# Kernel tuning notes

Measured on AMD Instinct MI355X. Metric: run time of the kernel, lower is better.

Reference implementation:

```python
import jax, jax.numpy as jnp
import numpy as np

PS = 2      # patch_size
TOPK = 3    # topk


def setup_inputs() -> dict:
    key = jax.random.key(0)
    x = jax.random.normal(key, (16, 128, 64, 64), dtype=jnp.float32)
    alpha = jnp.asarray(5.0, dtype=jnp.float32)
    return {"x": x, "alpha": alpha}


def reference(x, alpha):
    ps = PS
    b, c, h, w = x.shape
    nph, npw = h // ps, w // ps
    npatch = nph * npw
    pa = ps * ps
    # F.normalize(x, p=2, dim=-3): L2-normalize over channels
    nrm = jnp.sqrt(jnp.sum(x * x, axis=1, keepdims=True))
    x = x / jnp.maximum(nrm, 1e-12)
    # patchify: [b,c,h,w] -> [b,c,num_patches,patch_area]
    x = x.reshape(b * c * nph, ps, npw, ps)
    x = jnp.swapaxes(x, 1, 2).reshape(b, c, npatch, pa)
    diag = np.arange(ps) * (ps + 1)          # diagonal positions within a patch
    x = x[:, :, :, diag]                     # [b,c,npatch,ps]
    x = jnp.swapaxes(x, 1, 3)                # [b,ps,npatch,c]
    # per-diagonal-pixel patch correlation matrix
    corr = jnp.einsum('bpnc,bpmc->bpnm', x, x)           # [b,ps,np,np]
    avg = jnp.mean(corr, axis=1, keepdims=True)
    corr = jnp.concatenate([corr, avg], axis=1)          # [b,ps+1,np,np]
    # gaussian self-suppression mask (1 - gaussian centered at each patch)
    rat_s = 0.05
    sr, sc = nph * rat_s, npw * rat_s
    ind_r = jnp.arange(nph, dtype=jnp.float32).reshape(1, nph, 1)
    ind_c = jnp.arange(npw, dtype=jnp.float32).reshape(1, 1, npw)
    cr, cc = jnp.meshgrid(jnp.arange(nph, dtype=jnp.float32),
                          jnp.arange(npw, dtype=jnp.float32), indexing='ij')
    cent_r = cr.reshape(npatch, 1, 1)
    cent_c = cc.reshape(npatch, 1, 1)
    g = jnp.exp(-(ind_r - cent_r) ** 2 / (2.0 * sr * sr)) \
        * jnp.exp(-(ind_c - cent_c) ** 2 / (2.0 * sc * sc))   # [np,nph,npw]
    mask = (1.0 - g).reshape(1, 1, npatch, npatch)
    s = (corr * mask) * alpha
    # dual (row + column) softmax
    a = jax.nn.softmax(s, axis=-1) * jax.nn.softmax(s, axis=-2)  # [b,ps+1,np,np]
    # scatter: diagonal in-patch pixels get their own map, rest get the avg map
    src = np.full(pa, ps, dtype=np.int64)
    src[diag] = np.arange(ps)
    a = a[:, src]                              # [b,pa,np,np]
    # un-patchify attention back to [b, npatch, h, w]
    a = jnp.swapaxes(a, 1, 3)                  # [b,np,np,pa]
    a = a.reshape(b * npatch * nph, npw, ps, ps)
    a = jnp.swapaxes(a, 1, 2)
    a = a.reshape(b, npatch, h, w)
    # top-k over the patch (correlation-source) dim
    vals = jax.lax.top_k(jnp.moveaxis(a, 1, -1), TOPK)[0]  # [b,h,w,k]
    return jnp.moveaxis(vals, -1, 1)           # [b,k,h,w]
```

## Files before the change

### kernel.cpp

```cpp
#include <hip/hip_runtime.h>
#include <math.h>

#define NB 16
#define NCH 128
#define NH 64
#define NW 64
#define NP 1024

#define TN 32
#define TM 128
#define KC 32
#define KP 36
#define PK 40

#define NTILE 144

typedef __attribute__((ext_vector_type(8))) short short8v;
typedef __attribute__((ext_vector_type(4))) float f32x4;

__device__ __forceinline__ float med3(float a, float b, float c) {
  return __builtin_amdgcn_fmed3f(a, b, c);
}
__device__ __forceinline__ void top3_ins(float& t0, float& t1, float& t2, float a) {
  float n0 = fmaxf(t0, a);
  float n1 = med3(a, t0, t1);
  float n2 = med3(a, t1, t2);
  t0 = n0; t1 = n1; t2 = n2;
}
__device__ __forceinline__ float dot4(float4 a, float4 b) {
  return a.x * b.x + a.y * b.y + a.z * b.z + a.w * b.w;
}
__device__ __forceinline__ ushort f2bf(float f) {
  unsigned u = __float_as_uint(f);
  unsigned r = (u + 0x7FFFu + ((u >> 16) & 1u)) >> 16;
  return (ushort)r;
}
__device__ __forceinline__ float bf2f(ushort h) {
  return __uint_as_float(((unsigned)h) << 16);
}
__device__ __forceinline__ int tile_base(int g) {
  return 32 * g - 2 * g * (g - 1);
}

__global__ __launch_bounds__(256) void prep_split(const float* __restrict__ x,
                                                  ushort* __restrict__ Vs,
                                                  float* __restrict__ rsum) {
  int blk = blockIdx.x;
  int t = threadIdx.x;
  int gid = blk * 256 + t;
  if (gid < NB * 3 * NP) rsum[gid] = 0.f;

  int b = blk >> 5;
  int c = (blk >> 4) & 1;
  int ng = blk & 15;
  int nl = t >> 2;
  int kq = t & 3;
  int n = ng * 64 + nl;
  int i = 2 * (n >> 5) + c;
  int j = 2 * (n & 31) + c;
  const float* xp = x + (size_t)b * NCH * NH * NW + i * NW + j;

  float v[32];
#pragma unroll
  for (int e = 0; e < 32; ++e)
    v[e] = xp[(size_t)(kq * 32 + e) * NH * NW];

  float ss = 0.f;
#pragma unroll
  for (int e = 0; e < 32; ++e) ss += v[e] * v[e];
  ss += __shfl_xor(ss, 1, 64);
  ss += __shfl_xor(ss, 2, 64);
  float r = 1.0f / fmaxf(sqrtf(ss), 1e-12f);

  size_t base = ((size_t)(b * 2 + c) * 3) * NP * NCH + (size_t)n * NCH + kq * 32;
  ushort* p1 = Vs + base;
  ushort* p2 = Vs + base + (size_t)NP * NCH;
  ushort* p3 = Vs + base + (size_t)2 * NP * NCH;
#pragma unroll
  for (int kg2 = 0; kg2 < 4; ++kg2) {
    ushort h1[8], h2[8], h3[8];
#pragma unroll
    for (int e = 0; e < 8; ++e) {
      float vv = v[kg2 * 8 + e] * r;
      ushort a = f2bf(vv);
      float r1 = vv - bf2f(a);
      ushort bq = f2bf(r1);
      float r2 = r1 - bf2f(bq);
      ushort cq = f2bf(r2);
      h1[e] = a; h2[e] = bq; h3[e] = cq;
    }
    *(float4*)(p1 + kg2 * 8) = *(float4*)h1;
    *(float4*)(p2 + kg2 * 8) = *(float4*)h2;
    *(float4*)(p3 + kg2 * 8) = *(float4*)h3;
  }
}

__global__ __launch_bounds__(256, 4) void gemm_mfma(
    const ushort* __restrict__ Vs, const float* __restrict__ alpha_p,
    float2* __restrict__ Sbuf, float* __restrict__ rsum) {
  __shared__ __align__(16) char smem[3 * 32 * PK * 2 + 3 * 128 * PK * 2];
  ushort (*A_s)[32][PK] = reinterpret_cast<ushort(*)[32][PK]>(smem);
  ushort (*B_s)[128][PK] =
      reinterpret_cast<ushort(*)[128][PK]>(smem + 3 * 32 * PK * 2);

  int wg = blockIdx.x;
  int xcd = wg & 7;
  int jj = wg >> 3;
  int half = (jj >= NTILE) ? 1 : 0;
  const int b = 2 * xcd + half;
  int id = jj - half * NTILE;
  const int tid0 = id;
  int g = 0;
  while (id >= 4 * (8 - g)) { id -= 4 * (8 - g); ++g; }
  const int ni = 4 * g + id / (8 - g);
  const int mj = g + id % (8 - g);
  const int n0 = ni * TN;
  const int m0 = mj * TM;

  const int t = threadIdx.x;
  const int lane = t & 63, wv = t >> 6;
  const int jc = lane & 15, kg = lane >> 4;
  const float alpha = *alpha_p;
  const ushort* Vsb = Vs + (size_t)b * 6 * NP * NCH;
  float* rs = rsum + (size_t)b * 3 * NP;

  f32x4 acc[2][2][2];
#pragma unroll
  for (int c = 0; c < 2; ++c)
#pragma unroll
    for (int i = 0; i < 2; ++i)
#pragma unroll
      for (int j = 0; j < 2; ++j) acc[c][i][j] = (f32x4){0.f, 0.f, 0.f, 0.f};

#pragma unroll
  for (int c = 0; c < 2; ++c) {
    for (int k0 = 0; k0 < NCH; k0 += KC) {
      __syncthreads();
#pragma unroll
      for (int q = 0; q < 2; ++q) {
        int flat = q * 256 + t;
        if (flat < 384) {
          int p = flat >> 7;
          int rem = flat & 127;
          int row = rem >> 2, u = rem & 3;
          const ushort* src = Vsb + ((size_t)(c * 3 + p) * NP + n0 + row) * NCH + k0 + u * 8;
          *(float4*)&A_s[p][row][u * 8] = *(const float4*)src;
        }
      }
#pragma unroll
      for (int q = 0; q < 6; ++q) {
        int flat = q * 256 + t;
        int p = flat >> 9;
        int rem = flat & 511;
        int row = rem >> 2, u = rem & 3;
        const ushort* src = Vsb + ((size_t)(c * 3 + p) * NP + m0 + row) * NCH + k0 + u * 8;
        *(float4*)&B_s[p][row][u * 8] = *(const float4*)src;
      }
      __syncthreads();

      short8v a1n0 = *(const short8v*)&A_s[0][jc][kg * 8];
      short8v a1n1 = *(const short8v*)&A_s[0][16 + jc][kg * 8];
      short8v a2n0 = *(const short8v*)&A_s[1][jc][kg * 8];
      short8v a2n1 = *(const short8v*)&A_s[1][16 + jc][kg * 8];
      short8v a3n0 = *(const short8v*)&A_s[2][jc][kg * 8];
      short8v a3n1 = *(const short8v*)&A_s[2][16 + jc][kg * 8];
      {
        short8v b0 = *(const short8v*)&B_s[0][wv * 32 + jc][kg * 8];
        short8v b1 = *(const short8v*)&B_s[0][wv * 32 + 16 + jc][kg * 8];
        acc[c][0][0] = __builtin_amdgcn_mfma_f32_16x16x32_bf16(a1n0, b0, acc[c][0][0], 0, 0, 0);
        acc[c][1][0] = __builtin_amdgcn_mfma_f32_16x16x32_bf16(a1n1, b0, acc[c][1][0], 0, 0, 0);
        acc[c][0][1] = __builtin_amdgcn_mfma_f32_16x16x32_bf16(a1n0, b1, acc[c][0][1], 0, 0, 0);
        acc[c][1][1] = __builtin_amdgcn_mfma_f32_16x16x32_bf16(a1n1, b1, acc[c][1][1], 0, 0, 0);
        acc[c][0][0] = __builtin_amdgcn_mfma_f32_16x16x32_bf16(a2n0, b0, acc[c][0][0], 0, 0, 0);
        acc[c][1][0] = __builtin_amdgcn_mfma_f32_16x16x32_bf16(a2n1, b0, acc[c][1][0], 0, 0, 0);
        acc[c][0][1] = __builtin_amdgcn_mfma_f32_16x16x32_bf16(a2n0, b1, acc[c][0][1], 0, 0, 0);
        acc[c][1][1] = __builtin_amdgcn_mfma_f32_16x16x32_bf16(a2n1, b1, acc[c][1][1], 0, 0, 0);
        acc[c][0][0] = __builtin_amdgcn_mfma_f32_16x16x32_bf16(a3n0, b0, acc[c][0][0], 0, 0, 0);
        acc[c][1][0] = __builtin_amdgcn_mfma_f32_16x16x32_bf16(a3n1, b0, acc[c][1][0], 0, 0, 0);
        acc[c][0][1] = __builtin_amdgcn_mfma_f32_16x16x32_bf16(a3n0, b1, acc[c][0][1], 0, 0, 0);
        acc[c][1][1] = __builtin_amdgcn_mfma_f32_16x16x32_bf16(a3n1, b1, acc[c][1][1], 0, 0, 0);
      }
      {
        short8v b0 = *(const short8v*)&B_s[1][wv * 32 + jc][kg * 8];
        short8v b1 = *(const short8v*)&B_s[1][wv * 32 + 16 + jc][kg * 8];
        acc[c][0][0] = __builtin_amdgcn_mfma_f32_16x16x32_bf16(a1n0, b0, acc[c][0][0], 0, 0, 0);
        acc[c][1][0] = __builtin_amdgcn_mfma_f32_16x16x32_bf16(a1n1, b0, acc[c][1][0], 0, 0, 0);
        acc[c][0][1] = __builtin_amdgcn_mfma_f32_16x16x32_bf16(a1n0, b1, acc[c][0][1], 0, 0, 0);
        acc[c][1][1] = __builtin_amdgcn_mfma_f32_16x16x32_bf16(a1n1, b1, acc[c][1][1], 0, 0, 0);
        acc[c][0][0] = __builtin_amdgcn_mfma_f32_16x16x32_bf16(a2n0, b0, acc[c][0][0], 0, 0, 0);
        acc[c][1][0] = __builtin_amdgcn_mfma_f32_16x16x32_bf16(a2n1, b0, acc[c][1][0], 0, 0, 0);
        acc[c][0][1] = __builtin_amdgcn_mfma_f32_16x16x32_bf16(a2n0, b1, acc[c][0][1], 0, 0, 0);
        acc[c][1][1] = __builtin_amdgcn_mfma_f32_16x16x32_bf16(a2n1, b1, acc[c][1][1], 0, 0, 0);
      }
      {
        short8v b0 = *(const short8v*)&B_s[2][wv * 32 + jc][kg * 8];
        short8v b1 = *(const short8v*)&B_s[2][wv * 32 + 16 + jc][kg * 8];
        acc[c][0][0] = __builtin_amdgcn_mfma_f32_16x16x32_bf16(a1n0, b0, acc[c][0][0], 0, 0, 0);
        acc[c][1][0] = __builtin_amdgcn_mfma_f32_16x16x32_bf16(a1n1, b0, acc[c][1][0], 0, 0, 0);
        acc[c][0][1] = __builtin_amdgcn_mfma_f32_16x16x32_bf16(a1n0, b1, acc[c][0][1], 0, 0, 0);
        acc[c][1][1] = __builtin_amdgcn_mfma_f32_16x16x32_bf16(a1n1, b1, acc[c][1][1], 0, 0, 0);
      }
    }
  }

  float e[2][4][3];
  float gcol[2][3];
#pragma unroll
  for (int ns = 0; ns < 2; ++ns)
#pragma unroll
    for (int r = 0; r < 4; ++r)
#pragma unroll
      for (int c = 0; c < 3; ++c) e[ns][r][c] = 0.f;
#pragma unroll
  for (int ms = 0; ms < 2; ++ms)
#pragma unroll
    for (int c = 0; c < 3; ++c) gcol[ms][c] = 0.f;

#pragma unroll
  for (int ns = 0; ns < 2; ++ns) {
#pragma unroll
    for (int r = 0; r < 4; ++r) {
      int nl = ns * 16 + kg * 4 + r;
      int n = n0 + nl;
      int nr = n >> 5, nc = n & 31;
      float2* rowp = Sbuf + ((size_t)(b * NTILE + tid0) * 32 + nl) * TM;
#pragma unroll
      for (int ms = 0; ms < 2; ++ms) {
        int ml = wv * 32 + ms * 16 + jc;
        int m = m0 + ml;
        int dr = nr - (m >> 5);
        int dc = nc - (m & 31);
        float gss = __expf(-(float)(dr * dr + dc * dc) * 0.1953125f);
        float wgt = (1.0f - gss) * alpha;
        float s0 = acc[0][ns][ms][r] * wgt;
        float s1 = acc[1][ns][ms][r] * wgt;
        float e0 = __expf(s0);
        float e1 = __expf(s1);
        float e2 = __expf(0.5f * (s0 + s1));
        if (m >= n) {
          rowp[ml] = make_float2(s0, s1);
          e[ns][r][0] += e0; e[ns][r][1] += e1; e[ns][r][2] += e2;
        }
        if (m > n) { gcol[ms][0] += e0; gcol[ms][1] += e1; gcol[ms][2] += e2; }
      }
    }
  }
#pragma unroll
  for (int off = 1; off < 16; off <<= 1) {
#pragma unroll
    for (int ns = 0; ns < 2; ++ns)
#pragma unroll
      for (int r = 0; r < 4; ++r)
#pragma unroll
        for (int c = 0; c < 3; ++c)
          e[ns][r][c] += __shfl_xor(e[ns][r][c], off, 64);
  }
  if (jc == 0) {
#pragma unroll
    for (int ns = 0; ns < 2; ++ns)
#pragma unroll
      for (int r = 0; r < 4; ++r)
#pragma unroll
        for (int c = 0; c < 3; ++c)
          atomicAdd(&rs[(size_t)c * NP + (n0 + ns * 16 + kg * 4 + r)], e[ns][r][c]);
  }
#pragma unroll
  for (int off = 16; off < 64; off <<= 1) {
#pragma unroll
    for (int ms = 0; ms < 2; ++ms)
#pragma unroll
      for (int c = 0; c < 3; ++c)
        gcol[ms][c] += __shfl_xor(gcol[ms][c], off, 64);
  }
  if (kg == 0) {
#pragma unroll
    for (int ms = 0; ms < 2; ++ms) {
      int m = m0 + wv * 32 + ms * 16 + jc;
#pragma unroll
      for (int c = 0; c < 3; ++c)
        atomicAdd(&rs[(size_t)c * NP + m], gcol[ms][c]);
    }
  }
}

__global__ __launch_bounds__(256) void recip_kernel(float* __restrict__ p, int nelem) {
  int i = blockIdx.x * 256 + threadIdx.x;
  if (i < nelem) p[i] = 1.0f / p[i];
}

__global__ __launch_bounds__(256, 4) void tile_topk(
    const float2* __restrict__ Sbuf, const float* __restrict__ rinv,
    float* __restrict__ P) {
  __shared__ float2 tile[32][129];

  const int b = blockIdx.y;
  int id = blockIdx.x;
  const int tid0 = id;
  int g = 0;
  while (id >= 4 * (8 - g)) { id -= 4 * (8 - g); ++g; }
  const int ni = 4 * g + id / (8 - g);
  const int mj = g + id % (8 - g);
  const int n0 = ni * TN;
  const int m0 = mj * TM;

  const int t = threadIdx.x;
  const float* rb = rinv + (size_t)b * 3 * NP;
  const float2* src = Sbuf + (size_t)(b * NTILE + tid0) * 32 * TM;
  float* Pp = P + ((size_t)(b * NTILE + tid0) * 160) * 9;

#pragma unroll
  for (int q = 0; q < 16; ++q) {
    int flat = q * 256 + t;
    int row = flat >> 7;
    int colu = flat & 127;
    tile[row][colu] = src[row * TM + colu];
  }
  __syncthreads();

  {
    int rl = t >> 3;
    int c0 = (t & 7) * 16;
    int n = n0 + rl;
    float rin0 = rb[(size_t)0 * NP + n];
    float rin1 = rb[(size_t)1 * NP + n];
    float rin2 = rb[(size_t)2 * NP + n];
    float t0[3] = {0.f, 0.f, 0.f}, t1[3] = {0.f, 0.f, 0.f}, t2[3] = {0.f, 0.f, 0.f};
#pragma unroll
    for (int cc = 0; cc < 16; ++cc) {
      int ml = c0 + cc;
      int m = m0 + ml;
      if (m >= n) {
        float2 sv = tile[rl][ml];
        float a0 = __expf(2.0f * sv.x) * rin0 * rb[(size_t)0 * NP + m];
        float a1 = __expf(2.0f * sv.y) * rin1 * rb[(size_t)1 * NP + m];
        float a2 = __expf(sv.x + sv.y) * rin2 * rb[(size_t)2 * NP + m];
        top3_ins(t0[0], t1[0], t2[0], a0);
        top3_ins(t0[1], t1[1], t2[1], a1);
        top3_ins(t0[2], t1[2], t2[2], a2);
      }
    }
#pragma unroll
    for (int off = 1; off < 8; off <<= 1) {
#pragma unroll
      for (int c = 0; c < 3; ++c) {
        float o0 = __shfl_xor(t0[c], off, 64);
        float o1 = __shfl_xor(t1[c], off, 64);
        float o2 = __shfl_xor(t2[c], off, 64);
        top3_ins(t0[c], t1[c], t2[c], o0);
        top3_ins(t0[c], t1[c], t2[c], o1);
        top3_ins(t0[c], t1[c], t2[c], o2);
      }
    }
    if ((t & 7) == 0) {
#pragma unroll
      for (int c = 0; c < 3; ++c) {
        Pp[(size_t)rl * 9 + c * 3 + 0] = t0[c];
        Pp[(size_t)rl * 9 + c * 3 + 1] = t1[c];
        Pp[(size_t)rl * 9 + c * 3 + 2] = t2[c];
      }
    }
  }

  {
    int cu = t >> 1;
    int r0 = (t & 1) * 16;
    int m = m0 + cu;
    float rim0 = rb[(size_t)0 * NP + m];
    float rim1 = rb[(size_t)1 * NP + m];
    float rim2 = rb[(size_t)2 * NP + m];
    float t0[3] = {0.f, 0.f, 0.f}, t1[3] = {0.f, 0.f, 0.f}, t2[3] = {0.f, 0.f, 0.f};
#pragma unroll
    for (int rr = 0; rr < 16; ++rr) {
      int row = r0 + rr;
      int n = n0 + row;
      if (n < m) {
        float2 sv = tile[row][cu];
        float a0 = __expf(2.0f * sv.x) * rim0 * rb[(size_t)0 * NP + n];
        float a1 = __expf(2.0f * sv.y) * rim1 * rb[(size_t)1 * NP + n];
        float a2 = __expf(sv.x + sv.y) * rim2 * rb[(size_t)2 * NP + n];
        top3_ins(t0[0], t1[0], t2[0], a0);
        top3_ins(t0[1], t1[1], t2[1], a1);
        top3_ins(t0[2], t1[2], t2[2], a2);
      }
    }
#pragma unroll
    for (int c = 0; c < 3; ++c) {
      float o0 = __shfl_xor(t0[c], 1, 64);
      float o1 = __shfl_xor(t1[c], 1, 64);
      float o2 = __shfl_xor(t2[c], 1, 64);
      top3_ins(t0[c], t1[c], t2[c], o0);
      top3_ins(t0[c], t1[c], t2[c], o1);
      top3_ins(t0[c], t1[c], t2[c], o2);
    }
    if ((t & 1) == 0) {
#pragma unroll
      for (int c = 0; c < 3; ++c) {
        Pp[(size_t)(32 + cu) * 9 + c * 3 + 0] = t0[c];
        Pp[(size_t)(32 + cu) * 9 + c * 3 + 1] = t1[c];
        Pp[(size_t)(32 + cu) * 9 + c * 3 + 2] = t2[c];
      }
    }
  }
}

__global__ __launch_bounds__(256) void merge_kernel(
    const float* __restrict__ P, float* __restrict__ out) {
  int gid = blockIdx.x * 256 + threadIdx.x;
  int n = gid & (NP - 1);
  int tmp = gid >> 10;
  int c = tmp % 3;
  int b = tmp / 3;

  const float* Pb = P + (size_t)b * NTILE * 160 * 9;
  int g = n >> 7;
  int ni = n >> 5;
  int nl = n & 31;
  int ml = n & 127;

  float u0 = 0.f, u1 = 0.f, u2 = 0.f;
  int rbase = tile_base(g) + (ni - 4 * g) * (8 - g) - g;
  for (int mj = g; mj < 8; ++mj) {
    const float* p = Pb + ((size_t)(rbase + mj) * 160 + nl) * 9 + c * 3;
    top3_ins(u0, u1, u2, p[0]);
    top3_ins(u0, u1, u2, p[1]);
    top3_ins(u0, u1, u2, p[2]);
  }
  for (int nii = 0; nii <= 4 * g + 3; ++nii) {
    int gg = nii >> 2;
    int tid = tile_base(gg) + (nii - 4 * gg) * (8 - gg) + (g - gg);
    const float* p = Pb + ((size_t)tid * 160 + 32 + ml) * 9 + c * 3;
    top3_ins(u0, u1, u2, p[0]);
    top3_ins(u0, u1, u2, p[1]);
    top3_ins(u0, u1, u2, p[2]);
  }

  int pr = n >> 5, pc = n & 31;
  int ii0, jj0, ii1 = -1, jj1 = -1;
  if (c == 0)      { ii0 = 2 * pr;     jj0 = 2 * pc; }
  else if (c == 1) { ii0 = 2 * pr + 1; jj0 = 2 * pc + 1; }
  else             { ii0 = 2 * pr;     jj0 = 2 * pc + 1;
                     ii1 = 2 * pr + 1; jj1 = 2 * pc; }
  out[(((size_t)b * 3 + 0) * NH + ii0) * NW + jj0] = u0;
  out[(((size_t)b * 3 + 1) * NH + ii0) * NW + jj0] = u1;
  out[(((size_t)b * 3 + 2) * NH + ii0) * NW + jj0] = u2;
  if (ii1 >= 0) {
    out[(((size_t)b * 3 + 0) * NH + ii1) * NW + jj1] = u0;
    out[(((size_t)b * 3 + 1) * NH + ii1) * NW + jj1] = u1;
    out[(((size_t)b * 3 + 2) * NH + ii1) * NW + jj1] = u2;
  }
}

__global__ __launch_bounds__(256) void prep_kernel(const float* __restrict__ x,
                                                   float* __restrict__ V) {
  int blk = blockIdx.x;
  int t = threadIdx.x;
  int b = blk >> 3;
  int c = (blk >> 2) & 1;
  int n = (blk & 3) * 256 + t;
  int i = 2 * (n >> 5) + c;
  int j = 2 * (n & 31) + c;
  const float* xp = x + (size_t)b * NCH * NH * NW + i * NW + j;
  float ss = 0.f;
#pragma unroll 8
  for (int ch = 0; ch < NCH; ++ch) {
    float v = xp[(size_t)ch * NH * NW];
    ss += v * v;
  }
  float r = 1.0f / fmaxf(sqrtf(ss), 1e-12f);
  float* vp = V + (((size_t)b * 2 + c) * NP + n) * NCH;
#pragma unroll 8
  for (int ch = 0; ch < NCH; ++ch) {
    vp[ch] = xp[(size_t)ch * NH * NW] * r;
  }
}

template <int PASS>
__global__ __launch_bounds__(256, 2) void corr_kernel(
    const float* __restrict__ V, const float* __restrict__ alpha_p,
    float* __restrict__ rsum_g, float* __restrict__ out) {
  __shared__ __align__(16) float As[2][TN][KP];
  __shared__ __align__(16) float Bs[2][TM][KP];

  const int b = blockIdx.y;
  const int n0 = blockIdx.x * TN;
  const int t = threadIdx.x;
  const int tx = t & 31;
  const int ty = t >> 5;
  const float alpha = *alpha_p;
  const float* Vb = V + (size_t)b * 2 * NP * NCH;

  float sm[3][4];
  float t0[3][4], t1[3][4], t2[3][4];
  float rin[3][4];
#pragma unroll
  for (int c = 0; c < 3; ++c)
#pragma unroll
    for (int i = 0; i < 4; ++i) {
      sm[c][i] = 0.f;
      t0[c][i] = 0.f; t1[c][i] = 0.f; t2[c][i] = 0.f;
    }
  if (PASS == 2) {
#pragma unroll
    for (int c = 0; c < 3; ++c)
#pragma unroll
      for (int i = 0; i < 4; ++i) {
        int n = n0 + ty * 4 + i;
        rin[c][i] = 1.0f / rsum_g[((size_t)b * 3 + c) * NP + n];
      }
  }

  for (int mc = 0; mc < NP / TM; ++mc) {
    const int m0 = mc * TM;
    float acc[2][4][4];
#pragma unroll
    for (int c = 0; c < 2; ++c)
#pragma unroll
      for (int i = 0; i < 4; ++i)
#pragma unroll
        for (int j = 0; j < 4; ++j) acc[c][i][j] = 0.f;

    for (int k0 = 0; k0 < NCH; k0 += KC) {
      __syncthreads();
#pragma unroll
      for (int q = 0; q < 2; ++q) {
        int flat = q * 256 + t;
        int c = flat >> 8;
        int rem = flat & 255;
        int row = rem >> 3;
        int kgx = rem & 7;
        float4 v4 = *(const float4*)(Vb + ((size_t)c * NP + n0 + row) * NCH + k0 + kgx * 4);
        *(float4*)&As[c][row][kgx * 4] = v4;
      }
#pragma unroll
      for (int q = 0; q < 8; ++q) {
        int flat = q * 256 + t;
        int c = flat >> 10;
        int rem = flat & 1023;
        int row = rem >> 3;
        int kgx = rem & 7;
        float4 v4 = *(const float4*)(Vb + ((size_t)c * NP + m0 + row) * NCH + k0 + kgx * 4);
        *(float4*)&Bs[c][row][kgx * 4] = v4;
      }
      __syncthreads();

      for (int kgx = 0; kgx < KC; kgx += 4) {
        float4 a4[2][4], b4[2][4];
#pragma unroll
        for (int c = 0; c < 2; ++c)
#pragma unroll
          for (int i = 0; i < 4; ++i)
            a4[c][i] = *(const float4*)&As[c][ty * 4 + i][kgx];
#pragma unroll
        for (int c = 0; c < 2; ++c)
#pragma unroll
          for (int j = 0; j < 4; ++j)
            b4[c][j] = *(const float4*)&Bs[c][tx + 32 * j][kgx];
#pragma unroll
        for (int c = 0; c < 2; ++c)
#pragma unroll
          for (int i = 0; i < 4; ++i)
#pragma unroll
            for (int j = 0; j < 4; ++j)
              acc[c][i][j] += dot4(a4[c][i], b4[c][j]);
      }
    }

    float rim[3][4];
    if (PASS == 2) {
#pragma unroll
      for (int c = 0; c < 3; ++c)
#pragma unroll
        for (int j = 0; j < 4; ++j) {
          int m = m0 + tx + 32 * j;
          rim[c][j] = 1.0f / rsum_g[((size_t)b * 3 + c) * NP + m];
        }
    }
#pragma unroll
    for (int i = 0; i < 4; ++i) {
      int n = n0 + ty * 4 + i;
      int nr = n >> 5, nc = n & 31;
      float s[3][4];
#pragma unroll
      for (int j = 0; j < 4; ++j) {
        int m = m0 + tx + 32 * j;
        int dr = nr - (m >> 5);
        int dc = nc - (m & 31);
        float gq = __expf(-(float)(dr * dr + dc * dc) * 0.1953125f);
        float wgt = (1.0f - gq) * alpha;
        float s0v = acc[0][i][j] * wgt;
        float s1v = acc[1][i][j] * wgt;
        s[0][j] = s0v; s[1][j] = s1v; s[2][j] = 0.5f * (s0v + s1v);
      }
      if (PASS == 1) {
#pragma unroll
        for (int c = 0; c < 3; ++c) {
          sm[c][i] += __expf(s[c][0]) + __expf(s[c][1]) +
                      __expf(s[c][2]) + __expf(s[c][3]);
        }
      } else {
#pragma unroll
        for (int c = 0; c < 3; ++c) {
#pragma unroll
          for (int j = 0; j < 4; ++j) {
            float a = __expf(2.0f * s[c][j]) * rin[c][i] * rim[c][j];
            top3_ins(t0[c][i], t1[c][i], t2[c][i], a);
          }
        }
      }
    }
  }

  if (PASS == 1) {
#pragma unroll
    for (int off = 1; off < 32; off <<= 1) {
#pragma unroll
      for (int c = 0; c < 3; ++c)
#pragma unroll
        for (int i = 0; i < 4; ++i)
          sm[c][i] += __shfl_xor(sm[c][i], off, 64);
    }
    if (tx == 0) {
#pragma unroll
      for (int c = 0; c < 3; ++c)
#pragma unroll
        for (int i = 0; i < 4; ++i) {
          int n = n0 + ty * 4 + i;
          rsum_g[((size_t)b * 3 + c) * NP + n] = sm[c][i];
        }
    }
  } else {
#pragma unroll
    for (int off = 1; off < 32; off <<= 1) {
#pragma unroll
      for (int c = 0; c < 3; ++c)
#pragma unroll
        for (int i = 0; i < 4; ++i) {
          float o0 = __shfl_xor(t0[c][i], off, 64);
          float o1 = __shfl_xor(t1[c][i], off, 64);
          float o2 = __shfl_xor(t2[c][i], off, 64);
          top3_ins(t0[c][i], t1[c][i], t2[c][i], o0);
          top3_ins(t0[c][i], t1[c][i], t2[c][i], o1);
          top3_ins(t0[c][i], t1[c][i], t2[c][i], o2);
        }
    }
    if (tx == 0) {
#pragma unroll
      for (int c = 0; c < 3; ++c)
#pragma unroll
        for (int i = 0; i < 4; ++i) {
          int n = n0 + ty * 4 + i;
          int pr = n >> 5, pc = n & 31;
          float v0 = t0[c][i], v1 = t1[c][i], v2 = t2[c][i];
          int ii0, jj0, ii1 = -1, jj1 = -1;
          if (c == 0)      { ii0 = 2 * pr;     jj0 = 2 * pc; }
          else if (c == 1) { ii0 = 2 * pr + 1; jj0 = 2 * pc + 1; }
          else             { ii0 = 2 * pr;     jj0 = 2 * pc + 1;
                             ii1 = 2 * pr + 1; jj1 = 2 * pc; }
          out[(((size_t)b * 3 + 0) * NH + ii0) * NW + jj0] = v0;
          out[(((size_t)b * 3 + 1) * NH + ii0) * NW + jj0] = v1;
          out[(((size_t)b * 3 + 2) * NH + ii0) * NW + jj0] = v2;
          if (ii1 >= 0) {
            out[(((size_t)b * 3 + 0) * NH + ii1) * NW + jj1] = v0;
            out[(((size_t)b * 3 + 1) * NH + ii1) * NW + jj1] = v1;
            out[(((size_t)b * 3 + 2) * NH + ii1) * NW + jj1] = v2;
          }
        }
    }
  }
}

extern "C" void kernel_launch(void* const* d_in, const int* in_sizes, int n_in,
                              void* d_out, int out_size, void* d_ws, size_t ws_size,
                              hipStream_t stream) {
  const float* x = (const float*)d_in[0];
  const float* alpha = (const float*)d_in[1];
  float* out = (float*)d_out;

  const size_t nVsU = (size_t)NB * 6 * NP * NCH;
  const size_t nRs = (size_t)NB * 3 * NP;
  const size_t nSbuf = (size_t)NB * NTILE * 32 * TM;
  const size_t nP = (size_t)NB * NTILE * 160 * 9;

  ushort* Vs = (ushort*)d_ws;
  float* rsum = (float*)(Vs + nVsU);
  float2* Sbuf = (float2*)(rsum + nRs);
  float* P = (float*)(Sbuf + nSbuf);

  const size_t need_bytes = nVsU * 2 + nRs * 4 + nSbuf * 8 + nP * 4;

  if (ws_size >= need_bytes) {
    prep_split<<<512, 256, 0, stream>>>(x, Vs, rsum);
    gemm_mfma<<<NTILE * NB, 256, 0, stream>>>(Vs, alpha, Sbuf, rsum);
    recip_kernel<<<(NB * 3 * NP + 255) / 256, 256, 0, stream>>>(rsum, NB * 3 * NP);
    tile_topk<<<dim3(NTILE, NB), 256, 0, stream>>>(Sbuf, rsum, P);
    merge_kernel<<<(NB * 3 * NP) / 256, 256, 0, stream>>>(P, out);
  } else {
    float* V = (float*)d_ws;
    float* rsum_f = V + (size_t)NB * 2 * NP * NCH;
    prep_kernel<<<128, 256, 0, stream>>>(x, V);
    corr_kernel<1><<<dim3(NP / TN, NB), 256, 0, stream>>>(V, alpha, rsum_f, out);
    corr_kernel<2><<<dim3(NP / TN, NB), 256, 0, stream>>>(V, alpha, rsum_f, out);
  }
}
```

Before: 161.4 us.

## Compute attention values once per tile into shared memory before row/column top-3

Previously each tile element's exp and scaling was computed twice, once for the row top-3 pass and once for the column top-3 pass, with rinv read from global memory inside the loops. Now each element is computed once per channel into a shared-memory buffer, the rinv slices are staged in shared memory, and both reductions read from that buffer. The cost is extra shared memory (occupancy hint lowered from 4 to 3 blocks), three channel passes, and additional __syncthreads barriers.

```diff
diff --git a/kernel.cpp b/kernel.cpp
--- a/kernel.cpp
+++ b/kernel.cpp
@@ -288,10 +288,13 @@
   if (i < nelem) p[i] = 1.0f / p[i];
 }
 
-__global__ __launch_bounds__(256, 4) void tile_topk(
+__global__ __launch_bounds__(256, 3) void tile_topk(
     const float2* __restrict__ Sbuf, const float* __restrict__ rinv,
     float* __restrict__ P) {
-  __shared__ float2 tile[32][129];
+  __shared__ float2 tileS[32][129];
+  __shared__ float Ac[32][132];
+  __shared__ float rinL[3][32];
+  __shared__ float rimL[3][128];
 
   const int b = blockIdx.y;
   int id = blockIdx.x;
@@ -311,95 +314,74 @@
 #pragma unroll
   for (int q = 0; q < 16; ++q) {
     int flat = q * 256 + t;
-    int row = flat >> 7;
-    int colu = flat & 127;
-    tile[row][colu] = src[row * TM + colu];
+    tileS[flat >> 7][flat & 127] = src[flat];
+  }
+  if (t < 96) rinL[t >> 5][t & 31] = rb[(size_t)(t >> 5) * NP + n0 + (t & 31)];
+#pragma unroll
+  for (int q = 0; q < 2; ++q) {
+    int flat = q * 256 + t;
+    if (flat < 384)
+      rimL[flat >> 7][flat & 127] = rb[(size_t)(flat >> 7) * NP + m0 + (flat & 127)];
   }
   __syncthreads();
 
-  {
-    int rl = t >> 3;
-    int c0 = (t & 7) * 16;
-    int n = n0 + rl;
-    float rin0 = rb[(size_t)0 * NP + n];
-    float rin1 = rb[(size_t)1 * NP + n];
-    float rin2 = rb[(size_t)2 * NP + n];
-    float t0[3] = {0.f, 0.f, 0.f}, t1[3] = {0.f, 0.f, 0.f}, t2[3] = {0.f, 0.f, 0.f};
-#pragma unroll
-    for (int cc = 0; cc < 16; ++cc) {
-      int ml = c0 + cc;
-      int m = m0 + ml;
-      if (m >= n) {
-        float2 sv = tile[rl][ml];
-        float a0 = __expf(2.0f * sv.x) * rin0 * rb[(size_t)0 * NP + m];
-        float a1 = __expf(2.0f * sv.y) * rin1 * rb[(size_t)1 * NP + m];
-        float a2 = __expf(sv.x + sv.y) * rin2 * rb[(size_t)2 * NP + m];
-        top3_ins(t0[0], t1[0], t2[0], a0);
-        top3_ins(t0[1], t1[1], t2[1], a1);
-        top3_ins(t0[2], t1[2], t2[2], a2);
-      }
-    }
-#pragma unroll
-    for (int off = 1; off < 8; off <<= 1) {
-#pragma unroll
-      for (int c = 0; c < 3; ++c) {
-        float o0 = __shfl_xor(t0[c], off, 64);
-        float o1 = __shfl_xor(t1[c], off, 64);
-        float o2 = __shfl_xor(t2[c], off, 64);
-        top3_ins(t0[c], t1[c], t2[c], o0);
-        top3_ins(t0[c], t1[c], t2[c], o1);
-        top3_ins(t0[c], t1[c], t2[c], o2);
-      }
-    }
-    if ((t & 7) == 0) {
-#pragma unroll
-      for (int c = 0; c < 3; ++c) {
-        Pp[(size_t)rl * 9 + c * 3 + 0] = t0[c];
-        Pp[(size_t)rl * 9 + c * 3 + 1] = t1[c];
-        Pp[(size_t)rl * 9 + c * 3 + 2] = t2[c];
-      }
-    }
-  }
-
-  {
-    int cu = t >> 1;
-    int r0 = (t & 1) * 16;
-    int m = m0 + cu;
-    float rim0 = rb[(size_t)0 * NP + m];
-    float rim1 = rb[(size_t)1 * NP + m];
-    float rim2 = rb[(size_t)2 * NP + m];
-    float t0[3] = {0.f, 0.f, 0.f}, t1[3] = {0.f, 0.f, 0.f}, t2[3] = {0.f, 0.f, 0.f};
-#pragma unroll
-    for (int rr = 0; rr < 16; ++rr) {
-      int row = r0 + rr;
-      int n = n0 + row;
-      if (n < m) {
-        float2 sv = tile[row][cu];
-        float a0 = __expf(2.0f * sv.x) * rim0 * rb[(size_t)0 * NP + n];
-        float a1 = __expf(2.0f * sv.y) * rim1 * rb[(size_t)1 * NP + n];
-        float a2 = __expf(sv.x + sv.y) * rim2 * rb[(size_t)2 * NP + n];
-        top3_ins(t0[0], t1[0], t2[0], a0);
-        top3_ins(t0[1], t1[1], t2[1], a1);
-        top3_ins(t0[2], t1[2], t2[2], a2);
-      }
-    }
-#pragma unroll
-    for (int c = 0; c < 3; ++c) {
-      float o0 = __shfl_xor(t0[c], 1, 64);
-      float o1 = __shfl_xor(t1[c], 1, 64);
-      float o2 = __shfl_xor(t2[c], 1, 64);
-      top3_ins(t0[c], t1[c], t2[c], o0);
-      top3_ins(t0[c], t1[c], t2[c], o1);
-      top3_ins(t0[c], t1[c], t2[c], o2);
-    }
-    if ((t & 1) == 0) {
-#pragma unroll
-      for (int c = 0; c < 3; ++c) {
-        Pp[(size_t)(32 + cu) * 9 + c * 3 + 0] = t0[c];
-        Pp[(size_t)(32 + cu) * 9 + c * 3 + 1] = t1[c];
-        Pp[(size_t)(32 + cu) * 9 + c * 3 + 2] = t2[c];
-      }
-    }
+#pragma unroll
+  for (int c = 0; c < 3; ++c) {
+#pragma unroll
+    for (int q = 0; q < 16; ++q) {
+      int flat = q * 256 + t;
+      int row = flat >> 7, col = flat & 127;
+      int n = n0 + row, m = m0 + col;
+      float2 sv = tileS[row][col];
+      float s = (c == 0) ? sv.x : (c == 1) ? sv.y : 0.5f * (sv.x + sv.y);
+      float a = (m >= n) ? __expf(2.0f * s) * rinL[c][row] * rimL[c][col] : 0.f;
+      Ac[row][col] = a;
+    }
+    __syncthreads();
+
+    {
+      int rl = t >> 3, cs = t & 7;
+      float u0 = 0.f, u1 = 0.f, u2 = 0.f;
+#pragma unroll
+      for (int cc = 0; cc < 16; ++cc)
+        top3_ins(u0, u1, u2, Ac[rl][cs * 16 + cc]);
+#pragma unroll
+      for (int off = 1; off < 8; off <<= 1) {
+        float o0 = __shfl_xor(u0, off, 64);
+        float o1 = __shfl_xor(u1, off, 64);
+        float o2 = __shfl_xor(u2, off, 64);
+        top3_ins(u0, u1, u2, o0);
+        top3_ins(u0, u1, u2, o1);
+        top3_ins(u0, u1, u2, o2);
+      }
+      if (cs == 0) {
+        Pp[(size_t)rl * 9 + c * 3 + 0] = u0;
+        Pp[(size_t)rl * 9 + c * 3 + 1] = u1;
+        Pp[(size_t)rl * 9 + c * 3 + 2] = u2;
+      }
+    }
+    {
+      int cu = t >> 1, r0 = (t & 1) * 16;
+      int m = m0 + cu;
+      float u0 = 0.f, u1 = 0.f, u2 = 0.f;
+#pragma unroll
+      for (int rr = 0; rr < 16; ++rr) {
+        int row = r0 + rr;
+        if (n0 + row < m) top3_ins(u0, u1, u2, Ac[row][cu]);
+      }
+      float o0 = __shfl_xor(u0, 1, 64);
+      float o1 = __shfl_xor(u1, 1, 64);
+      float o2 = __shfl_xor(u2, 1, 64);
+      top3_ins(u0, u1, u2, o0);
+      top3_ins(u0, u1, u2, o1);
+      top3_ins(u0, u1, u2, o2);
+      if ((t & 1) == 0) {
+        Pp[(size_t)(32 + cu) * 9 + c * 3 + 0] = u0;
+        Pp[(size_t)(32 + cu) * 9 + c * 3 + 1] = u1;
+        Pp[(size_t)(32 + cu) * 9 + c * 3 + 2] = u2;
+      }
+    }
+    __syncthreads();
   }
 }
 
```

After: 145.5 us, median of 2. 9.8% less time.
